# Performance work log

Hardware: AMD Instinct MI355X
Metric: run time of the kernel (lower is better)

## Reference

```python
import jax, jax.numpy as jnp
import numpy as np

F_IN = 512
N_STAGES = 6
BATCH = 16384


def entmax15_1d(v):
    # Exact entmax with alpha=1.5 on a 1D vector (Peters et al. 2019).
    x = (v - jnp.max(v)) * 0.5
    xs = jnp.sort(x)[::-1]                      # descending
    rho = jnp.arange(1, xs.shape[0] + 1, dtype=xs.dtype)
    mean = jnp.cumsum(xs) / rho
    mean_sq = jnp.cumsum(xs * xs) / rho
    ss = rho * (mean_sq - mean * mean)
    delta = jnp.clip((1.0 - ss) / rho, 0.0, None)
    tau = mean - jnp.sqrt(delta)
    support_size = jnp.sum(tau <= xs)
    tau_star = tau[support_size - 1]
    return jnp.square(jnp.clip(x - tau_star, 0.0, None))


def setup_inputs() -> dict:
    key = jax.random.key(0)
    ks = jax.random.split(key, 7)
    F2 = 2 * F_IN
    lim_in = 1.0 / np.sqrt(F2)   # torch Linear default init bound (fan_in = 2F)
    x = jax.random.normal(ks[0], (BATCH, F_IN), dtype=jnp.float32)
    masks = jax.random.uniform(ks[1], (N_STAGES, F_IN), dtype=jnp.float32)  # Beta-sampled in torch; uniform(0,1) is in-range
    Win_w = jax.random.uniform(ks[2], (N_STAGES, F2, F2), minval=-lim_in, maxval=lim_in, dtype=jnp.float32)
    Win_b = jax.random.uniform(ks[3], (N_STAGES, F2), minval=-lim_in, maxval=lim_in, dtype=jnp.float32)
    Wout_w = jax.random.uniform(ks[4], (N_STAGES, F_IN, F2), minval=-lim_in, maxval=lim_in, dtype=jnp.float32)
    Wout_b = jax.random.uniform(ks[5], (N_STAGES, F_IN), minval=-lim_in, maxval=lim_in, dtype=jnp.float32)
    return {"x": x, "masks": masks, "Win_w": Win_w, "Win_b": Win_b,
            "Wout_w": Wout_w, "Wout_b": Wout_b}


def reference(x, masks, Win_w, Win_b, Wout_w, Wout_b):
    F = x.shape[-1]
    h = x
    for d in range(N_STAGES):
        feature = entmax15_1d(masks[d]) * x                      # [B, F]
        h_in = jnp.concatenate([feature, h], axis=-1) @ Win_w[d].T + Win_b[d]  # [B, 2F]
        z = jax.nn.sigmoid(h_in[:, :F])
        r = jax.nn.sigmoid(h_in[:, F:])
        h_out = jnp.tanh(jnp.concatenate([r * h, x], axis=-1) @ Wout_w[d].T + Wout_b[d])
        h = (1.0 - z) * h + z * h_out                            # dropout p=0 -> identity
    return h
```

## Files before the change

### kernel.cpp

```cpp
#include <hip/hip_runtime.h>
#include <stdint.h>
#include <math.h>

typedef unsigned short u16;
typedef short s16x8 __attribute__((ext_vector_type(8)));
typedef float f32x4 __attribute__((ext_vector_type(4)));
typedef u16 u16x4 __attribute__((ext_vector_type(4)));

#define FDIM 512
#define F2 1024
#define BATCH 16384
#define NST 6
#define KDIM 1024
#define NT 32

__device__ __forceinline__ u16 f2bf(float f) {
  uint32_t u = __float_as_uint(f);
  u += 0x7FFFu + ((u >> 16) & 1u);
  return (u16)(u >> 16);
}
__device__ __forceinline__ float bf2f(u16 b) {
  return __uint_as_float((uint32_t)b << 16);
}

#define LOG2E 1.44269504f
__device__ __forceinline__ float fast_sigmoid(float v) {
  float e = __builtin_amdgcn_exp2f(-v * LOG2E);
  return __builtin_amdgcn_rcpf(1.0f + e);
}
__device__ __forceinline__ float fast_tanh(float v) {
  float e = __builtin_amdgcn_exp2f(v * (2.0f * LOG2E));
  return 1.0f - 2.0f * __builtin_amdgcn_rcpf(1.0f + e);
}

__device__ __forceinline__ void ld_lds16(u16* lds, const u16* g) {
  __builtin_amdgcn_global_load_lds(
      (const __attribute__((address_space(1))) uint32_t*)g,
      (__attribute__((address_space(3))) uint32_t*)lds, 16, 0, 0);
}

__global__ __launch_bounds__(512) void entmax_kernel(const float* __restrict__ masks,
                                                     float* __restrict__ fm) {
  __shared__ float sx[FDIM];
  __shared__ float ssort[FDIM];
  __shared__ float stau[FDIM];
  __shared__ float2 sc[2][FDIM];
  const int d = blockIdx.x;
  const int j = threadIdx.x;
  float v = masks[d * FDIM + j];

  stau[j] = v;
  __syncthreads();
  for (int s = 256; s > 0; s >>= 1) {
    if (j < s) stau[j] = fmaxf(stau[j], stau[j + s]);
    __syncthreads();
  }
  float mx = stau[0];
  __syncthreads();

  float xx = (v - mx) * 0.5f;
  sx[j] = xx;
  __syncthreads();

  int r = 0;
  const float4* sx4 = (const float4*)sx;
#pragma unroll 4
  for (int i4 = 0; i4 < FDIM / 4; i4++) {
    float4 q = sx4[i4];
    int i = i4 << 2;
    r += (q.x > xx) || (q.x == xx && (i + 0) < j);
    r += (q.y > xx) || (q.y == xx && (i + 1) < j);
    r += (q.z > xx) || (q.z == xx && (i + 2) < j);
    r += (q.w > xx) || (q.w == xx && (i + 3) < j);
  }
  ssort[r] = xx;
  __syncthreads();
  float xs = ssort[j];

  sc[0][j] = make_float2(xs, xs * xs);
  __syncthreads();
  int pp = 0;
  for (int off = 1; off < FDIM; off <<= 1) {
    float2 t = sc[pp][j];
    if (j >= off) {
      float2 u = sc[pp][j - off];
      t.x += u.x;
      t.y += u.y;
    }
    sc[pp ^ 1][j] = t;
    __syncthreads();
    pp ^= 1;
  }
  float2 cs = sc[pp][j];

  float rho = (float)(j + 1);
  float mean = cs.x / rho;
  float msq = cs.y / rho;
  float ss = rho * (msq - mean * mean);
  float delta = (1.f - ss) / rho;
  if (delta < 0.f) delta = 0.f;
  float tau = mean - sqrtf(delta);
  stau[j] = tau;
  int cnt = __syncthreads_count(tau <= xs);
  float tstar = stau[cnt - 1];
  float c = fmaxf(xx - tstar, 0.f);
  fm[d * FDIM + j] = c * c;
}

__global__ __launch_bounds__(256) void cvt_w1_kernel(const float* __restrict__ src,
                                                     const float* __restrict__ fm,
                                                     u16* __restrict__ dst) {
  int t = blockIdx.x * 256 + threadIdx.x;
  int k = (t & 255) << 2;
  int dn = t >> 8;
  int d = dn >> 10;
  float4 v = *(const float4*)(src + (size_t)t * 4);
  if (k < FDIM) {
    float4 s = *(const float4*)(fm + (size_t)d * FDIM + k);
    v.x *= s.x; v.y *= s.y; v.z *= s.z; v.w *= s.w;
  }
  u16x4 o = {f2bf(v.x), f2bf(v.y), f2bf(v.z), f2bf(v.w)};
  *(u16x4*)(dst + (size_t)t * 4) = o;
}

#define N4_W2 (NST * FDIM * F2 / 4)
__global__ __launch_bounds__(256) void prep_kernel(const float* __restrict__ W2f,
                                                   u16* __restrict__ W2b,
                                                   const float* __restrict__ x,
                                                   u16* __restrict__ A1,
                                                   u16* __restrict__ A2) {
  int t = blockIdx.x * 256 + threadIdx.x;
  if (t < N4_W2) {
    float4 v = *(const float4*)(W2f + (size_t)t * 4);
    u16x4 o = {f2bf(v.x), f2bf(v.y), f2bf(v.z), f2bf(v.w)};
    *(u16x4*)(W2b + (size_t)t * 4) = o;
  } else {
    int u = t - N4_W2;
    int m = u >> 7;
    int c = (u & 127) << 2;
    float4 xv = *(const float4*)(x + (size_t)m * FDIM + c);
    u16x4 o = {f2bf(xv.x), f2bf(xv.y), f2bf(xv.z), f2bf(xv.w)};
    *(u16x4*)(A1 + (size_t)m * F2 + c) = o;
    *(u16x4*)(A1 + (size_t)m * F2 + FDIM + c) = o;
    *(u16x4*)(A2 + (size_t)m * F2 + FDIM + c) = o;
  }
}

__device__ __forceinline__ void gemm_core128(const u16* __restrict__ Ag,
                                             const u16* __restrict__ Bg,
                                             int m0, int n0, u16* smem,
                                             f32x4 acc[4][4]) {
  const int tid = threadIdx.x;
  const int lane = tid & 63;
  const int wid = tid >> 6;
  const int wm = wid >> 1;
  const int wn = wid & 1;

  const int rs = tid >> 2;
  const int colsw = ((tid & 3) ^ ((rs >> 1) & 3)) << 3;
  const u16* gA0 = Ag + (size_t)(m0 + rs) * KDIM + colsw;
  const u16* gA1 = gA0 + (size_t)64 * KDIM;
  const u16* gB0 = Bg + (size_t)(n0 + rs) * KDIM + colsw;
  const u16* gB1 = gB0 + (size_t)64 * KDIM;
  const int lds_u = tid * 8;

  const int fcs = ((lane >> 4) ^ ((lane >> 1) & 3)) << 3;
  const int aoff = (wm * 64 + (lane & 15)) * 32 + fcs;
  const int boff = 4096 + (wn * 64 + (lane & 15)) * 32 + fcs;

#pragma unroll
  for (int i = 0; i < 4; i++)
#pragma unroll
    for (int j = 0; j < 4; j++) acc[i][j] = (f32x4){0.f, 0.f, 0.f, 0.f};

#pragma unroll
  for (int kt = 0; kt < 3; kt++) {
    u16* rb = smem + kt * 8192;
    ld_lds16(rb + lds_u, gA0 + kt * 32);
    ld_lds16(rb + 2048 + lds_u, gA1 + kt * 32);
    ld_lds16(rb + 4096 + lds_u, gB0 + kt * 32);
    ld_lds16(rb + 6144 + lds_u, gB1 + kt * 32);
  }
  asm volatile("s_waitcnt vmcnt(8)" ::: "memory");
  __builtin_amdgcn_s_barrier();
  __builtin_amdgcn_sched_barrier(0);

  for (int t = 0; t < NT; t++) {
    const u16* rb = smem + (t & 3) * 8192;
    u16* sb = smem + ((t + 3) & 3) * 8192;
    if (t + 3 < NT) {
      const int k0 = (t + 3) * 32;
      ld_lds16(sb + lds_u, gA0 + k0);
      ld_lds16(sb + 2048 + lds_u, gA1 + k0);
      ld_lds16(sb + 4096 + lds_u, gB0 + k0);
      ld_lds16(sb + 6144 + lds_u, gB1 + k0);
    }
    s16x8 af[4], bfr[4];
#pragma unroll
    for (int f = 0; f < 4; f++)
      af[f] = *(const s16x8*)(rb + aoff + f * 512);
#pragma unroll
    for (int g = 0; g < 4; g++)
      bfr[g] = *(const s16x8*)(rb + boff + g * 512);
    if (t < NT - 3) {
      asm volatile("s_waitcnt vmcnt(8)" ::: "memory");
    } else if (t == NT - 3) {
      asm volatile("s_waitcnt vmcnt(4)" ::: "memory");
    } else if (t == NT - 2) {
      asm volatile("s_waitcnt vmcnt(0)" ::: "memory");
    }
    __builtin_amdgcn_s_setprio(1);
#pragma unroll
    for (int f = 0; f < 4; f++)
#pragma unroll
      for (int g = 0; g < 4; g++)
        acc[f][g] = __builtin_amdgcn_mfma_f32_16x16x32_bf16(af[f], bfr[g], acc[f][g], 0, 0, 0);
    __builtin_amdgcn_s_setprio(0);
    __builtin_amdgcn_sched_barrier(0);
    __builtin_amdgcn_s_barrier();
    __builtin_amdgcn_sched_barrier(0);
  }
}

__device__ __forceinline__ void gemm_core4(const u16* __restrict__ Ag,
                                           const u16* __restrict__ Bg,
                                           int m0, int n0, u16* smem,
                                           f32x4 acc[4][4]) {
  const int tid = threadIdx.x;
  const int lane = tid & 63;
  const int wid = tid >> 6;
  const int wm = wid >> 2;
  const int wn = wid & 3;

  const int rs = tid >> 2;
  const int colsw = ((tid & 3) ^ ((rs >> 1) & 3)) << 3;
  const u16* gA0 = Ag + (size_t)(m0 + rs) * KDIM + colsw;
  const u16* gB0 = Bg + (size_t)(n0 + rs) * KDIM + colsw;
  const u16* gB1 = gB0 + (size_t)128 * KDIM;
  const int lds_u = tid * 8;

  const int fcs = ((lane >> 4) ^ ((lane >> 1) & 3)) << 3;
  const int aoff = (wm * 64 + (lane & 15)) * 32 + fcs;
  const int boff = (wn * 64 + (lane & 15)) * 32 + fcs;

#pragma unroll
  for (int i = 0; i < 4; i++)
#pragma unroll
    for (int j = 0; j < 4; j++) acc[i][j] = (f32x4){0.f, 0.f, 0.f, 0.f};

#pragma unroll
  for (int kt = 0; kt < 3; kt++) {
    u16* rb = smem + kt * 12288;
    ld_lds16(rb + lds_u, gA0 + kt * 32);
    ld_lds16(rb + 4096 + lds_u, gB0 + kt * 32);
    ld_lds16(rb + 8192 + lds_u, gB1 + kt * 32);
  }
  asm volatile("s_waitcnt vmcnt(6)" ::: "memory");
  __builtin_amdgcn_s_barrier();
  __builtin_amdgcn_sched_barrier(0);

  for (int t = 0; t < NT; t++) {
    const u16* rb = smem + (t & 3) * 12288;
    u16* sb = smem + ((t + 3) & 3) * 12288;
    if (t + 3 < NT) {
      ld_lds16(sb + lds_u, gA0 + (t + 3) * 32);
      ld_lds16(sb + 4096 + lds_u, gB0 + (t + 3) * 32);
      ld_lds16(sb + 8192 + lds_u, gB1 + (t + 3) * 32);
    }
    s16x8 af[4], bfr[4];
#pragma unroll
    for (int f = 0; f < 4; f++)
      af[f] = *(const s16x8*)(rb + aoff + f * 512);
#pragma unroll
    for (int g = 0; g < 4; g++)
      bfr[g] = *(const s16x8*)(rb + 4096 + boff + g * 512);
    if (t < NT - 3) {
      asm volatile("s_waitcnt vmcnt(6)" ::: "memory");
    } else if (t == NT - 3) {
      asm volatile("s_waitcnt vmcnt(3)" ::: "memory");
    } else if (t == NT - 2) {
      asm volatile("s_waitcnt vmcnt(0)" ::: "memory");
    }
    __builtin_amdgcn_s_setprio(1);
#pragma unroll
    for (int f = 0; f < 4; f++)
#pragma unroll
      for (int g = 0; g < 4; g++)
        acc[f][g] = __builtin_amdgcn_mfma_f32_16x16x32_bf16(af[f], bfr[g], acc[f][g], 0, 0, 0);
    __builtin_amdgcn_s_setprio(0);
    __builtin_amdgcn_sched_barrier(0);
    __builtin_amdgcn_s_barrier();
    __builtin_amdgcn_sched_barrier(0);
  }
}

__global__ __launch_bounds__(256, 2) void gemm1_kernel(const u16* __restrict__ A1,
                                                       const u16* __restrict__ W1,
                                                       const float* __restrict__ b1,
                                                       _Float16* __restrict__ zbuf,
                                                       u16* __restrict__ A2) {
  __shared__ u16 smem[32768];
  const int bx = blockIdx.x;
  const int wg = (bx & 7) * 128 + (bx >> 3);
  const int m0 = (wg >> 3) << 7;
  const int n0 = (wg & 7) << 7;
  f32x4 acc[4][4];
  gemm_core128(A1, W1, m0, n0, smem, acc);

  const int lane = threadIdx.x & 63;
  const int wid = threadIdx.x >> 6;
  const int wm = wid >> 1;
  const int wn = wid & 1;
  const int fcol = lane & 15;
  const int frow = (lane >> 4) << 2;

  if (n0 < FDIM) {
#pragma unroll
    for (int f = 0; f < 4; f++)
#pragma unroll
      for (int g = 0; g < 4; g++)
#pragma unroll
        for (int r = 0; r < 4; r++) {
          int gm = m0 + wm * 64 + f * 16 + frow + r;
          int gn = n0 + wn * 64 + g * 16 + fcol;
          float v = acc[f][g][r] + b1[gn];
          zbuf[(size_t)gm * FDIM + gn] = (_Float16)fast_sigmoid(v);
        }
  } else {
#pragma unroll
    for (int f = 0; f < 4; f++)
#pragma unroll
      for (int g = 0; g < 4; g++)
#pragma unroll
        for (int r = 0; r < 4; r++) {
          int gm = m0 + wm * 64 + f * 16 + frow + r;
          int gn = n0 + wn * 64 + g * 16 + fcol;
          float v = acc[f][g][r] + b1[gn];
          float s = fast_sigmoid(v);
          int c = gn - FDIM;
          float h = bf2f(A1[(size_t)gm * F2 + FDIM + c]);
          A2[(size_t)gm * F2 + c] = f2bf(s * h);
        }
  }
}

__global__ __launch_bounds__(512, 2) void gemm2_kernel(const u16* __restrict__ A2,
                                                       const u16* __restrict__ W2,
                                                       const float* __restrict__ b2,
                                                       const _Float16* __restrict__ zbuf,
                                                       u16* __restrict__ A1,
                                                       float* __restrict__ out,
                                                       int last) {
  __shared__ u16 smem[49152];
  const int bx = blockIdx.x;
  const int wg = (bx & 7) * 32 + (bx >> 3);
  const int m0 = (wg >> 1) << 7;
  const int n0 = (wg & 1) << 8;
  f32x4 acc[4][4];
  gemm_core4(A2, W2, m0, n0, smem, acc);

  const int lane = threadIdx.x & 63;
  const int wid = threadIdx.x >> 6;
  const int wm = wid >> 2;
  const int wn = wid & 3;
  const int fcol = lane & 15;
  const int frow = (lane >> 4) << 2;

#pragma unroll
  for (int f = 0; f < 4; f++)
#pragma unroll
    for (int g = 0; g < 4; g++)
#pragma unroll
      for (int r = 0; r < 4; r++) {
        int gm = m0 + wm * 64 + f * 16 + frow + r;
        int gn = n0 + wn * 64 + g * 16 + fcol;
        float v = acc[f][g][r] + b2[gn];
        float ho = fast_tanh(v);
        size_t idx = (size_t)gm * FDIM + gn;
        float z = (float)zbuf[idx];
        float hv = bf2f(A1[(size_t)gm * F2 + FDIM + gn]);
        float hn = (1.0f - z) * hv + z * ho;
        if (last)
          out[idx] = hn;
        else
          A1[(size_t)gm * F2 + FDIM + gn] = f2bf(hn);
      }
}

extern "C" void kernel_launch(void* const* d_in, const int* in_sizes, int n_in,
                              void* d_out, int out_size, void* d_ws, size_t ws_size,
                              hipStream_t stream) {
  (void)in_sizes; (void)n_in; (void)out_size; (void)ws_size;
  const float* x = (const float*)d_in[0];
  const float* masks = (const float*)d_in[1];
  const float* W1f = (const float*)d_in[2];
  const float* b1 = (const float*)d_in[3];
  const float* W2f = (const float*)d_in[4];
  const float* b2 = (const float*)d_in[5];

  char* ws = (char*)d_ws;
  float* fm = (float*)ws;       ws += (size_t)NST * FDIM * 4;
  u16* W1b = (u16*)ws;          ws += (size_t)NST * F2 * F2 * 2;
  u16* W2b = (u16*)ws;          ws += (size_t)NST * FDIM * F2 * 2;
  u16* A1 = (u16*)ws;           ws += (size_t)BATCH * F2 * 2;
  u16* A2 = (u16*)ws;           ws += (size_t)BATCH * F2 * 2;
  _Float16* zbuf = (_Float16*)ws; ws += (size_t)BATCH * FDIM * 2;
  float* out = (float*)d_out;

  entmax_kernel<<<NST, 512, 0, stream>>>(masks, fm);
  cvt_w1_kernel<<<NST * F2 * F2 / 4 / 256, 256, 0, stream>>>(W1f, fm, W1b);
  {
    int total = N4_W2 + BATCH * 128;
    prep_kernel<<<(total + 255) / 256, 256, 0, stream>>>(W2f, W2b, x, A1, A2);
  }

  for (int d = 0; d < NST; d++) {
    gemm1_kernel<<<(BATCH / 128) * (F2 / 128), 256, 0, stream>>>(
        A1, W1b + (size_t)d * F2 * F2, b1 + d * F2, zbuf, A2);
    gemm2_kernel<<<(BATCH / 128) * (FDIM / 256), 512, 0, stream>>>(
        A2, W2b + (size_t)d * FDIM * F2, b2 + d * FDIM, zbuf,
        A1, out, d == NST - 1);
  }
}
```

Baseline: 531.9 us.

## Rewrite gemm1 with 256x128 tiles, K=64 steps and a quarter-phased 3-stage pipeline

Replaces the 128x128 gemm1 core with a 512-thread kernel that computes 256x128 output tiles using 64-wide K steps. Tiles move through a three-slot LDS ring buffer with a new XOR swizzle. Each K step is split into four quadrant phases, and global-to-LDS staging loads are spread across those phases so they overlap with MFMA work. The larger tile raises operand reuse and cuts global traffic per FLOP, at the cost of about 144KB of LDS per block, which limits occupancy to one block per CU, and more barriers per K step.

New measurement: 522.9 us. About the same (-1.7%).

```diff
diff --git a/kernel.cpp b/kernel.cpp
--- a/kernel.cpp
+++ b/kernel.cpp
@@ -13,6 +13,7 @@
 #define NST 6
 #define KDIM 1024
 #define NT 32
+#define NKT 16
 
 __device__ __forceinline__ u16 f2bf(float f) {
   uint32_t u = __float_as_uint(f);
@@ -146,79 +147,155 @@
   }
 }
 
-__device__ __forceinline__ void gemm_core128(const u16* __restrict__ Ag,
-                                             const u16* __restrict__ Bg,
-                                             int m0, int n0, u16* smem,
-                                             f32x4 acc[4][4]) {
+__global__ __launch_bounds__(512, 2) void gemm1_kernel(const u16* __restrict__ A1,
+                                                       const u16* __restrict__ W1,
+                                                       const float* __restrict__ b1,
+                                                       _Float16* __restrict__ zbuf,
+                                                       u16* __restrict__ A2) {
+  __shared__ u16 smem[73728];
+  const int bx = blockIdx.x;
+  const int wg = (bx & 7) * 64 + (bx >> 3);
+  const int m0 = (wg >> 3) << 8;
+  const int n0 = (wg & 7) << 7;
+
   const int tid = threadIdx.x;
   const int lane = tid & 63;
   const int wid = tid >> 6;
   const int wm = wid >> 1;
   const int wn = wid & 1;
-
-  const int rs = tid >> 2;
-  const int colsw = ((tid & 3) ^ ((rs >> 1) & 3)) << 3;
-  const u16* gA0 = Ag + (size_t)(m0 + rs) * KDIM + colsw;
-  const u16* gA1 = gA0 + (size_t)64 * KDIM;
-  const u16* gB0 = Bg + (size_t)(n0 + rs) * KDIM + colsw;
-  const u16* gB1 = gB0 + (size_t)64 * KDIM;
-  const int lds_u = tid * 8;
-
-  const int fcs = ((lane >> 4) ^ ((lane >> 1) & 3)) << 3;
-  const int aoff = (wm * 64 + (lane & 15)) * 32 + fcs;
-  const int boff = 4096 + (wn * 64 + (lane & 15)) * 32 + fcs;
-
+  const int l15 = lane & 15;
+  const int kg = lane >> 4;
+
+  const int csrc = ((tid & 7) ^ ((tid >> 3) & 7)) << 3;
+  const u16* gA = A1 + (size_t)(m0 + (tid >> 3)) * KDIM + csrc;
+  const u16* gB = W1 + (size_t)(n0 + (tid >> 3)) * KDIM + csrc;
+  const int ldst = tid * 8;
+
+  int cA0 = ((0 * 4 + kg) ^ (l15 & 7)) << 3;
+  int cA1 = ((1 * 4 + kg) ^ (l15 & 7)) << 3;
+  const int rowbaseA = (wm >> 1) * 8192 + ((wm & 1) * 64 + l15) * 64;
+  const int rowbaseB = 16384 + (wn * 64 + l15) * 64;
+
+  f32x4 acc[4][4];
 #pragma unroll
   for (int i = 0; i < 4; i++)
 #pragma unroll
     for (int j = 0; j < 4; j++) acc[i][j] = (f32x4){0.f, 0.f, 0.f, 0.f};
 
 #pragma unroll
-  for (int kt = 0; kt < 3; kt++) {
-    u16* rb = smem + kt * 8192;
-    ld_lds16(rb + lds_u, gA0 + kt * 32);
-    ld_lds16(rb + 2048 + lds_u, gA1 + kt * 32);
-    ld_lds16(rb + 4096 + lds_u, gB0 + kt * 32);
-    ld_lds16(rb + 6144 + lds_u, gB1 + kt * 32);
-  }
-  asm volatile("s_waitcnt vmcnt(8)" ::: "memory");
+  for (int jj = 0; jj < 2; jj++) {
+    u16* sb = smem + jj * 24576;
+    const u16* ga = gA + jj * 64;
+    const u16* gb = gB + jj * 64;
+    ld_lds16(sb + ldst, ga);
+    ld_lds16(sb + 4096 + ldst, ga + (size_t)64 * KDIM);
+    ld_lds16(sb + 8192 + ldst, ga + (size_t)128 * KDIM);
+    ld_lds16(sb + 12288 + ldst, ga + (size_t)192 * KDIM);
+    ld_lds16(sb + 16384 + ldst, gb);
+    ld_lds16(sb + 20480 + ldst, gb + (size_t)64 * KDIM);
+  }
+  asm volatile("s_waitcnt vmcnt(6)" ::: "memory");
   __builtin_amdgcn_s_barrier();
   __builtin_amdgcn_sched_barrier(0);
 
-  for (int t = 0; t < NT; t++) {
-    const u16* rb = smem + (t & 3) * 8192;
-    u16* sb = smem + ((t + 3) & 3) * 8192;
-    if (t + 3 < NT) {
-      const int k0 = (t + 3) * 32;
-      ld_lds16(sb + lds_u, gA0 + k0);
-      ld_lds16(sb + 2048 + lds_u, gA1 + k0);
-      ld_lds16(sb + 4096 + lds_u, gB0 + k0);
-      ld_lds16(sb + 6144 + lds_u, gB1 + k0);
+  s16x8 afq[2][2], bfq[2][2];
+
+  int slot = 0, sslot = 2;
+  for (int j = 0; j < NKT; j++) {
+    const u16* rb = smem + slot * 24576;
+    u16* sb = smem + sslot * 24576;
+    const int js = j + 2;
+    const u16* ga = gA + js * 64;
+    const u16* gb = gB + js * 64;
+    const bool do_stage = (js < NKT);
+
+#pragma unroll
+    for (int q = 0; q < 4; q++) {
+      const int mh = (q >> 1);
+      const int nh = (q == 1 || q == 2);
+      if (q == 0 || q == 2) {
+#pragma unroll
+        for (int i = 0; i < 2; i++) {
+          afq[i][0] = *(const s16x8*)(rb + rowbaseA + (mh * 2 + i) * 1024 + cA0);
+          afq[i][1] = *(const s16x8*)(rb + rowbaseA + (mh * 2 + i) * 1024 + cA1);
+        }
+      }
+      if (q != 2) {
+#pragma unroll
+        for (int n = 0; n < 2; n++) {
+          bfq[n][0] = *(const s16x8*)(rb + rowbaseB + (nh * 2 + n) * 1024 + cA0);
+          bfq[n][1] = *(const s16x8*)(rb + rowbaseB + (nh * 2 + n) * 1024 + cA1);
+        }
+      }
+      if (do_stage) {
+        if (q == 0) {
+          ld_lds16(sb + ldst, ga);
+          ld_lds16(sb + 4096 + ldst, ga + (size_t)64 * KDIM);
+        } else if (q == 1) {
+          ld_lds16(sb + 8192 + ldst, ga + (size_t)128 * KDIM);
+          ld_lds16(sb + 12288 + ldst, ga + (size_t)192 * KDIM);
+        } else if (q == 2) {
+          ld_lds16(sb + 16384 + ldst, gb);
+          ld_lds16(sb + 20480 + ldst, gb + (size_t)64 * KDIM);
+        }
+      }
+      __builtin_amdgcn_s_barrier();
+      asm volatile("s_waitcnt lgkmcnt(0)" ::: "memory");
+      __builtin_amdgcn_sched_barrier(0);
+      __builtin_amdgcn_s_setprio(1);
+#pragma unroll
+      for (int s = 0; s < 2; s++)
+#pragma unroll
+        for (int i = 0; i < 2; i++)
+#pragma unroll
+          for (int n = 0; n < 2; n++)
+            acc[mh * 2 + i][nh * 2 + n] = __builtin_amdgcn_mfma_f32_16x16x32_bf16(
+                afq[i][s], bfq[n][s], acc[mh * 2 + i][nh * 2 + n], 0, 0, 0);
+      __builtin_amdgcn_s_setprio(0);
+      __builtin_amdgcn_sched_barrier(0);
+      if (q == 3) {
+        if (j <= 13) {
+          asm volatile("s_waitcnt vmcnt(6)" ::: "memory");
+        } else if (j == 14) {
+          asm volatile("s_waitcnt vmcnt(0)" ::: "memory");
+        }
+      }
+      __builtin_amdgcn_s_barrier();
+      __builtin_amdgcn_sched_barrier(0);
     }
-    s16x8 af[4], bfr[4];
+    slot = (slot == 2) ? 0 : slot + 1;
+    sslot = (sslot == 2) ? 0 : sslot + 1;
+  }
+
+  const int fcol = l15;
+  const int frow = kg << 2;
+  if (n0 < FDIM) {
 #pragma unroll
     for (int f = 0; f < 4; f++)
-      af[f] = *(const s16x8*)(rb + aoff + f * 512);
-#pragma unroll
-    for (int g = 0; g < 4; g++)
-      bfr[g] = *(const s16x8*)(rb + boff + g * 512);
-    if (t < NT - 3) {
-      asm volatile("s_waitcnt vmcnt(8)" ::: "memory");
-    } else if (t == NT - 3) {
-      asm volatile("s_waitcnt vmcnt(4)" ::: "memory");
-    } else if (t == NT - 2) {
-      asm volatile("s_waitcnt vmcnt(0)" ::: "memory");
-    }
-    __builtin_amdgcn_s_setprio(1);
+#pragma unroll
+      for (int g = 0; g < 4; g++)
+#pragma unroll
+        for (int r = 0; r < 4; r++) {
+          int gm = m0 + wm * 64 + f * 16 + frow + r;
+          int gn = n0 + wn * 64 + g * 16 + fcol;
+          float v = acc[f][g][r] + b1[gn];
+          zbuf[(size_t)gm * FDIM + gn] = (_Float16)fast_sigmoid(v);
+        }
+  } else {
 #pragma unroll
     for (int f = 0; f < 4; f++)
 #pragma unroll
       for (int g = 0; g < 4; g++)
-        acc[f][g] = __builtin_amdgcn_mfma_f32_16x16x32_bf16(af[f], bfr[g], acc[f][g], 0, 0, 0);
-    __builtin_amdgcn_s_setprio(0);
-    __builtin_amdgcn_sched_barrier(0);
-    __builtin_amdgcn_s_barrier();
-    __builtin_amdgcn_sched_barrier(0);
+#pragma unroll
+        for (int r = 0; r < 4; r++) {
+          int gm = m0 + wm * 64 + f * 16 + frow + r;
+          int gn = n0 + wn * 64 + g * 16 + fcol;
+          float v = acc[f][g][r] + b1[gn];
+          float s = fast_sigmoid(v);
+          int c = gn - FDIM;
+          float h = bf2f(A1[(size_t)gm * F2 + FDIM + c]);
+          A2[(size_t)gm * F2 + c] = f2bf(s * h);
+        }
   }
 }
 
@@ -291,56 +368,6 @@
     __builtin_amdgcn_sched_barrier(0);
     __builtin_amdgcn_s_barrier();
     __builtin_amdgcn_sched_barrier(0);
-  }
-}
-
-__global__ __launch_bounds__(256, 2) void gemm1_kernel(const u16* __restrict__ A1,
-                                                       const u16* __restrict__ W1,
-                                                       const float* __restrict__ b1,
-                                                       _Float16* __restrict__ zbuf,
-                                                       u16* __restrict__ A2) {
-  __shared__ u16 smem[32768];
-  const int bx = blockIdx.x;
-  const int wg = (bx & 7) * 128 + (bx >> 3);
-  const int m0 = (wg >> 3) << 7;
-  const int n0 = (wg & 7) << 7;
-  f32x4 acc[4][4];
-  gemm_core128(A1, W1, m0, n0, smem, acc);
-
-  const int lane = threadIdx.x & 63;
-  const int wid = threadIdx.x >> 6;
-  const int wm = wid >> 1;
-  const int wn = wid & 1;
-  const int fcol = lane & 15;
-  const int frow = (lane >> 4) << 2;
-
-  if (n0 < FDIM) {
-#pragma unroll
-    for (int f = 0; f < 4; f++)
-#pragma unroll
-      for (int g = 0; g < 4; g++)
-#pragma unroll
-        for (int r = 0; r < 4; r++) {
-          int gm = m0 + wm * 64 + f * 16 + frow + r;
-          int gn = n0 + wn * 64 + g * 16 + fcol;
-          float v = acc[f][g][r] + b1[gn];
-          zbuf[(size_t)gm * FDIM + gn] = (_Float16)fast_sigmoid(v);
-        }
-  } else {
-#pragma unroll
-    for (int f = 0; f < 4; f++)
-#pragma unroll
-      for (int g = 0; g < 4; g++)
-#pragma unroll
-        for (int r = 0; r < 4; r++) {
-          int gm = m0 + wm * 64 + f * 16 + frow + r;
-          int gn = n0 + wn * 64 + g * 16 + fcol;
-          float v = acc[f][g][r] + b1[gn];
-          float s = fast_sigmoid(v);
-          int c = gn - FDIM;
-          float h = bf2f(A1[(size_t)gm * F2 + FDIM + c]);
-          A2[(size_t)gm * F2 + c] = f2bf(s * h);
-        }
   }
 }
 
@@ -415,7 +442,7 @@
   }
 
   for (int d = 0; d < NST; d++) {
-    gemm1_kernel<<<(BATCH / 128) * (F2 / 128), 256, 0, stream>>>(
+    gemm1_kernel<<<(BATCH / 256) * (F2 / 128), 512, 0, stream>>>(
         A1, W1b + (size_t)d * F2 * F2, b1 + d * F2, zbuf, A2);
     gemm2_kernel<<<(BATCH / 128) * (FDIM / 256), 512, 0, stream>>>(
         A2, W2b + (size_t)d * FDIM * F2, b2 + d * FDIM, zbuf,
```
